# Performance work log

Hardware: AMD Instinct MI355X
Metric: run time of the kernel (lower is better)

Reference implementation:

```python
import jax, jax.numpy as jnp
import numpy as np

B, S, D = 2, 2048, 1024
H = 16
HD = D // H
SCALE = HD ** (-0.5)


def setup_inputs() -> dict:
    key = jax.random.key(0)
    k1, k2, k3, k4 = jax.random.split(key, 4)
    x = jax.random.normal(k1, (B, S, D), dtype=jnp.float32)
    # nn.Linear-style init scale to keep activations sane
    w_qkv = jax.random.normal(k2, (3 * D, D), dtype=jnp.float32) * (D ** -0.5)
    w_out = jax.random.normal(k3, (D, D), dtype=jnp.float32) * (D ** -0.5)
    b_out = jax.random.normal(k4, (D,), dtype=jnp.float32) * 0.01
    return {"x": x, "w_qkv": w_qkv, "w_out": w_out, "b_out": b_out}


def reference(x, w_qkv, w_out, b_out):
    b, s, d = x.shape
    # qkv projection (no bias): [b, s, 3d]
    qkv = jnp.einsum('bsd,ed->bse', x, w_qkv)
    # Rearrange 'b c (e h hd) -> e b h c hd'
    qkv = qkv.reshape(b, s, 3, H, HD).transpose(2, 0, 3, 1, 4)
    # NOTE: original splits as (v, q, k) in that order
    v, q, k = qkv[0], qkv[1], qkv[2]
    # scale applied after matmul, as in the original
    scores = jnp.einsum('bhqd,bhkd->bhqk', q, k) * SCALE
    attn = jax.nn.softmax(scores, axis=-1)
    o = jnp.einsum('bhqk,bhkd->bhqd', attn, v)
    # 'b h c hd -> b c (h hd)'
    o = o.transpose(0, 2, 1, 3).reshape(b, s, d)
    return jnp.einsum('bsd,ed->bse', o, w_out) + b_out
```

## Files before the change

kernel.cpp:

```cpp
#include <hip/hip_runtime.h>
#include <cstdint>
#include <cstddef>

#define BB 2
#define SS 2048
#define DD 1024
#define HH 16
#define HDIM 64

typedef short bf16x8 __attribute__((ext_vector_type(8)));
typedef short bf16x4 __attribute__((ext_vector_type(4)));
typedef float f32x4 __attribute__((ext_vector_type(4)));
typedef float f32x2 __attribute__((ext_vector_type(2)));

union U4S8 { uint4 u; bf16x8 s; };
union U2S4 { uint2 u; bf16x4 s; unsigned short h[4]; };

#if defined(__HIP_DEVICE_COMPILE__)
# if __has_builtin(__builtin_amdgcn_mfma_f32_16x16x16bf16_1k)
#  define MFMA_PV(a, b, c) __builtin_amdgcn_mfma_f32_16x16x16bf16_1k((a), (b), (c), 0, 0, 0)
# else
#  define MFMA_PV(a, b, c) __builtin_amdgcn_mfma_f32_16x16x16_bf16((a), (b), (c), 0, 0, 0)
# endif
# if __has_builtin(__builtin_amdgcn_exp2f)
#  define EXP2(x) __builtin_amdgcn_exp2f(x)
# else
#  define EXP2(x) exp2f(x)
# endif
#else
# define MFMA_PV(a, b, c) (c)
# define EXP2(x) exp2f(x)
#endif

__device__ __forceinline__ unsigned short f2bf(float f) {
    union { float f; unsigned int u; } c; c.f = f;
    unsigned int u = c.u;
    unsigned int r = (u + 0x7FFFu + ((u >> 16) & 1u)) >> 16;
    return (unsigned short)r;
}

__device__ __forceinline__ void async_cp16(const void* g, void* l) {
    __builtin_amdgcn_global_load_lds(
        (const __attribute__((address_space(1))) void*)g,
        (__attribute__((address_space(3))) void*)l, 16, 0, 0);
}

__global__ __launch_bounds__(256) void cvt_all(
    const float* __restrict__ x, const float* __restrict__ wq,
    const float* __restrict__ wo,
    unsigned short* __restrict__ xb, unsigned short* __restrict__ wqb,
    unsigned short* __restrict__ wob) {
    int i = blockIdx.x * 256 + threadIdx.x;
    const float* in; unsigned short* out; int j;
    if (i < 524288)       { in = x;  out = xb;  j = i; }
    else if (i < 917504)  { in = wq; out = wqb; j = i - 524288; }
    else                  { in = wo; out = wob; j = i - 917504; }
    float4 a = ((const float4*)in)[2 * j];
    float4 b = ((const float4*)in)[2 * j + 1];
    union { uint4 u; unsigned short h[8]; } o;
    o.h[0] = f2bf(a.x); o.h[1] = f2bf(a.y); o.h[2] = f2bf(a.z); o.h[3] = f2bf(a.w);
    o.h[4] = f2bf(b.x); o.h[5] = f2bf(b.y); o.h[6] = f2bf(b.z); o.h[7] = f2bf(b.w);
    ((uint4*)out)[j] = o.u;
}

__global__ __launch_bounds__(256) void gemm_qkv(
    const unsigned short* __restrict__ A,
    const unsigned short* __restrict__ Bw,
    unsigned short* __restrict__ qb, unsigned short* __restrict__ kb,
    unsigned short* __restrict__ vb) {
    const int K = 1024;
    __shared__ unsigned short smem[18432];
    int tid = threadIdx.x;
    int lane = tid & 63, wave = tid >> 6;
    int wm = (wave & 1) * 64, wn = (wave >> 1) * 64;
    int m0 = blockIdx.y * 128, n0 = blockIdx.x * 128;
    int lm = lane & 15, lq = lane >> 4;

    f32x4 acc[4][4] = {};

    int sdst = tid * 8;
    const unsigned short* gA = A  + (size_t)(m0 + (tid >> 2)) * K + (tid & 3) * 8;
    const unsigned short* gB = Bw + (size_t)(n0 + (tid >> 2)) * K + (tid & 3) * 8;

#define GSTAGE(k0, buf) do {                                          \
        async_cp16(gA + (k0),          smem + (buf) + sdst);          \
        async_cp16(gA + 64 * K + (k0), smem + (buf) + 2048 + sdst);   \
        async_cp16(gB + (k0),          smem + (buf) + 4096 + sdst);   \
        async_cp16(gB + 64 * K + (k0), smem + (buf) + 6144 + sdst);   \
    } while (0)

    GSTAGE(0, 0);
    for (int k0 = 0; k0 < K; k0 += 64) {
        #pragma unroll
        for (int hf = 0; hf < 2; hf++) {
            int base = hf ? 8192 : 0;
            int obuf = hf ? 0 : 8192;
            __syncthreads();
            int kn = k0 + 32 + hf * 32;
            if (kn < K) GSTAGE(kn, obuf);
            const unsigned short* As = smem + base;
            const unsigned short* Bs = smem + base + 4096;
            U4S8 af[4], bfx[4];
            #pragma unroll
            for (int i = 0; i < 4; i++) {
                af[i].u  = *(const uint4*)(As + (wm + i * 16 + lm) * 32 + lq * 8);
                bfx[i].u = *(const uint4*)(Bs + (wn + i * 16 + lm) * 32 + lq * 8);
            }
            #pragma unroll
            for (int mi = 0; mi < 4; mi++)
                #pragma unroll
                for (int ni = 0; ni < 4; ni++)
                    acc[mi][ni] = __builtin_amdgcn_mfma_f32_16x16x32_bf16(
                        af[mi].s, bfx[ni].s, acc[mi][ni], 0, 0, 0);
        }
    }
#undef GSTAGE
    __syncthreads();

    unsigned short* Lw = smem + wave * 4608;
    int b = m0 >> 11;
    int s_base = (m0 + wm) & 2047;
    if (n0 < 1024) {
        int h = (n0 + wn) >> 6;
        #pragma unroll
        for (int mi = 0; mi < 4; mi++)
            #pragma unroll
            for (int ni = 0; ni < 4; ni++)
                #pragma unroll
                for (int r = 0; r < 4; r++)
                    Lw[(ni * 16 + lm) * 72 + mi * 16 + lq * 4 + r] =
                        f2bf(acc[mi][ni][r]);
        __builtin_amdgcn_wave_barrier();
        unsigned short* vdst = vb + ((size_t)(b * HH + h) * HDIM) * SS + s_base;
        #pragma unroll
        for (int it = 0; it < 8; it++) {
            int hd = it * 8 + (lane >> 3);
            int so = (lane & 7) * 8;
            uint4 val = *(const uint4*)&Lw[hd * 72 + so];
            *(uint4*)(vdst + (size_t)hd * SS + so) = val;
        }
    } else {
        bool isq = n0 < 2048;
        unsigned short* dst = isq ? qb : kb;
        float scale = isq ? 0.18033688f : 1.0f;
        int h = ((n0 + wn) >> 6) & 15;
        #pragma unroll
        for (int mi = 0; mi < 4; mi++)
            #pragma unroll
            for (int ni = 0; ni < 4; ni++)
                #pragma unroll
                for (int r = 0; r < 4; r++)
                    Lw[(mi * 16 + lq * 4 + r) * 72 + ni * 16 + lm] =
                        f2bf(acc[mi][ni][r] * scale);
        __builtin_amdgcn_wave_barrier();
        unsigned short* qdst =
            dst + ((size_t)(b * HH + h) * SS + s_base) * HDIM;
        #pragma unroll
        for (int it = 0; it < 8; it++) {
            int srw = it * 8 + (lane >> 3);
            int so = (lane & 7) * 8;
            uint4 val = *(const uint4*)&Lw[srw * 72 + so];
            *(uint4*)(qdst + (size_t)srw * HDIM + so) = val;
        }
    }
}

__global__ __launch_bounds__(256) void attn(
    const unsigned short* __restrict__ qb,
    const unsigned short* __restrict__ kb,
    const unsigned short* __restrict__ vb,
    unsigned short* __restrict__ ob) {
    int bh = blockIdx.y;
    int q0 = blockIdx.x * 64;
    int tid = threadIdx.x, lane = tid & 63, wave = tid >> 6;
    int lm = lane & 15, lq = lane >> 4;

    __shared__ unsigned short smem[4 * 4096];

    const unsigned short* qg = qb + (size_t)bh * SS * HDIM;
    const unsigned short* kg = kb + (size_t)bh * SS * HDIM;
    const unsigned short* vg = vb + (size_t)bh * HDIM * SS;

    U4S8 qf[2];
    #pragma unroll
    for (int ks = 0; ks < 2; ks++)
        qf[ks].u = *(const uint4*)(
            qg + (size_t)(q0 + wave * 16 + lm) * HDIM + ks * 32 + lq * 8);

    f32x4 oacc[4] = {};
    f32x2 lsum2 = {0.f, 0.f};

    int lm7 = lm & 7;
    int kidx = lm * 64 + 8 * (lq ^ lm7);
    int vidx[4];
    #pragma unroll
    for (int kc = 0; kc < 4; kc++)
        vidx[kc] = lm * 64 + 8 * (((kc << 1) | (lq >> 1)) ^ lm7) + (lq & 1) * 4;

    int srow = tid >> 3;
    int scl  = (tid & 7) ^ (srow & 7);
    int sdst = tid * 8;
    const unsigned short* kptr = kg + (size_t)srow * HDIM + scl * 8;
    const unsigned short* vptr = vg + (size_t)srow * SS + scl * 8;

    #define STAGE(buf)                                                         \
        do {                                                                   \
            async_cp16(kptr,             smem + (buf) + sdst);                 \
            async_cp16(kptr + 32 * HDIM, smem + (buf) + 2048 + sdst);          \
            async_cp16(vptr,             smem + (buf) + 4096 + sdst);          \
            async_cp16(vptr + 32 * SS,   smem + (buf) + 6144 + sdst);          \
            kptr += 64 * HDIM; vptr += 64;                                     \
        } while (0)

    STAGE(0);

    for (int kt = 0; kt < SS / 64; kt += 2) {
        #pragma unroll
        for (int hf = 0; hf < 2; hf++) {
            int base = hf ? 8192 : 0;
            int obuf = hf ? 0 : 8192;
            __syncthreads();
            STAGE(obuf);

            U2S4 pb[4];
            #pragma unroll
            for (int mi = 0; mi < 4; mi++) {
                U4S8 kf0, kf1;
                kf0.u = *(const uint4*)(smem + base + mi * 1024 + kidx);
                kf1.u = *(const uint4*)(smem + base + mi * 1024 + (kidx ^ 32));
                f32x4 sa = {};
                sa = __builtin_amdgcn_mfma_f32_16x16x32_bf16(kf0.s, qf[0].s, sa, 0, 0, 0);
                sa = __builtin_amdgcn_mfma_f32_16x16x32_bf16(kf1.s, qf[1].s, sa, 0, 0, 0);
                float p0 = EXP2(sa[0]);
                float p1 = EXP2(sa[1]);
                float p2 = EXP2(sa[2]);
                float p3 = EXP2(sa[3]);
                f32x2 a01; a01[0] = p0; a01[1] = p1;
                f32x2 a23; a23[0] = p2; a23[1] = p3;
                lsum2 += a01;
                lsum2 += a23;
                unsigned int b0 = __float_as_uint(p0) + 0x8000u;
                unsigned int b1 = __float_as_uint(p1) + 0x8000u;
                unsigned int b2 = __float_as_uint(p2) + 0x8000u;
                unsigned int b3 = __float_as_uint(p3) + 0x8000u;
                pb[mi].u.x = __builtin_amdgcn_perm(b1, b0, 0x07060302u);
                pb[mi].u.y = __builtin_amdgcn_perm(b3, b2, 0x07060302u);
            }

            #pragma unroll
            for (int mi2 = 0; mi2 < 4; mi2++) {
                #pragma unroll
                for (int kc = 0; kc < 4; kc++) {
                    U2S4 vf;
                    vf.u = *(const uint2*)(smem + base + 4096 + mi2 * 1024 + vidx[kc]);
                    oacc[mi2] = MFMA_PV(vf.s, pb[kc].s, oacc[mi2]);
                }
            }
        }
    }
    #undef STAGE

    float s = lsum2[0] + lsum2[1];
    s += __shfl_xor(s, 16);
    s += __shfl_xor(s, 32);
    float inv = 1.f / s;

    __syncthreads();
    unsigned short* Ow = smem + wave * (16 * 72);
    #pragma unroll
    for (int mi2 = 0; mi2 < 4; mi2++) {
        U2S4 t;
        #pragma unroll
        for (int r = 0; r < 4; r++)
            t.h[r] = f2bf(oacc[mi2][r] * inv);
        *(uint2*)&Ow[lm * 72 + mi2 * 16 + lq * 4] = t.u;
    }
    __builtin_amdgcn_wave_barrier();
    int b = bh >> 4, h = bh & 15;
    #pragma unroll
    for (int it = 0; it < 2; it++) {
        int q  = it * 8 + (lane >> 3);
        int off = (lane & 7) * 8;
        uint4 val = *(const uint4*)&Ow[q * 72 + off];
        int srw = q0 + wave * 16 + q;
        *(uint4*)(ob + (size_t)(b * SS + srw) * DD + h * 64 + off) = val;
    }
}

__global__ __launch_bounds__(256) void gemm_out(
    const unsigned short* __restrict__ A,
    const unsigned short* __restrict__ Bw,
    const float* __restrict__ bias, float* __restrict__ out) {
    const int K = 1024;
    __shared__ unsigned short smem[12288];
    int tid = threadIdx.x;
    int lane = tid & 63, wave = tid >> 6;
    int wm = (wave & 1) * 64, wn = (wave >> 1) * 32;
    int m0 = blockIdx.y * 128, n0 = blockIdx.x * 64;
    int lm = lane & 15, lq = lane >> 4;

    f32x4 acc[4][2] = {};

    int sdst = tid * 8;
    const unsigned short* gA = A  + (size_t)(m0 + (tid >> 2)) * K + (tid & 3) * 8;
    const unsigned short* gB = Bw + (size_t)(n0 + (tid >> 2)) * K + (tid & 3) * 8;

#define OSTAGE(k0, buf) do {                                          \
        async_cp16(gA + (k0),          smem + (buf) + sdst);          \
        async_cp16(gA + 64 * K + (k0), smem + (buf) + 2048 + sdst);   \
        async_cp16(gB + (k0),          smem + (buf) + 4096 + sdst);   \
    } while (0)

    OSTAGE(0, 0);
    for (int k0 = 0; k0 < K; k0 += 64) {
        #pragma unroll
        for (int hf = 0; hf < 2; hf++) {
            int base = hf ? 6144 : 0;
            int obuf = hf ? 0 : 6144;
            __syncthreads();
            int kn = k0 + 32 + hf * 32;
            if (kn < K) OSTAGE(kn, obuf);
            const unsigned short* As = smem + base;
            const unsigned short* Bs = smem + base + 4096;
            U4S8 af[4], bfx[2];
            #pragma unroll
            for (int i = 0; i < 4; i++)
                af[i].u = *(const uint4*)(As + (wm + i * 16 + lm) * 32 + lq * 8);
            #pragma unroll
            for (int i = 0; i < 2; i++)
                bfx[i].u = *(const uint4*)(Bs + (wn + i * 16 + lm) * 32 + lq * 8);
            #pragma unroll
            for (int mi = 0; mi < 4; mi++)
                #pragma unroll
                for (int ni = 0; ni < 2; ni++)
                    acc[mi][ni] = __builtin_amdgcn_mfma_f32_16x16x32_bf16(
                        af[mi].s, bfx[ni].s, acc[mi][ni], 0, 0, 0);
        }
    }
#undef OSTAGE

    #pragma unroll
    for (int mi = 0; mi < 4; mi++) {
        int gr = m0 + wm + mi * 16 + lq * 4;
        #pragma unroll
        for (int ni = 0; ni < 2; ni++) {
            int gc = n0 + wn + ni * 16 + lm;
            float bv = bias[gc];
            #pragma unroll
            for (int r = 0; r < 4; r++)
                out[(size_t)(gr + r) * DD + gc] = acc[mi][ni][r] + bv;
        }
    }
}

extern "C" void kernel_launch(void* const* d_in, const int* in_sizes, int n_in,
                              void* d_out, int out_size, void* d_ws, size_t ws_size,
                              hipStream_t stream) {
    const float* x     = (const float*)d_in[0];
    const float* w_qkv = (const float*)d_in[1];
    const float* w_out = (const float*)d_in[2];
    const float* b_out = (const float*)d_in[3];
    float* out = (float*)d_out;

    unsigned short* ws = (unsigned short*)d_ws;
    const size_t NX = (size_t)BB * SS * DD;
    unsigned short* x_bf    = ws;
    unsigned short* wqkv_bf = x_bf + NX;
    unsigned short* wout_bf = wqkv_bf + 3145728;
    unsigned short* q_buf   = wout_bf + 1048576;
    unsigned short* k_buf   = q_buf + NX;
    unsigned short* v_buf   = k_buf + NX;
    unsigned short* o_buf   = v_buf + NX;

    cvt_all<<<4096, 256, 0, stream>>>(x, w_qkv, w_out, x_bf, wqkv_bf, wout_bf);
    gemm_qkv<<<dim3(24, 32), 256, 0, stream>>>(x_bf, wqkv_bf, q_buf, k_buf, v_buf);
    attn<<<dim3(32, 32), 256, 0, stream>>>(q_buf, k_buf, v_buf, o_buf);
    gemm_out<<<dim3(16, 32), 256, 0, stream>>>(o_buf, wout_bf, b_out, out);
}
```

Baseline: 206.6 us.

## Process two query tiles per wave in attention to reuse K/V fragments

Each attention block now covers 128 queries instead of 64, with every wave owning two 16-row query tiles. The K and V fragments loaded from shared memory are reused for both tiles, so the global K/V staging traffic and the LDS reads per query are halved. The grid shrinks to 512 blocks. The cost is more accumulator and probability registers per thread, which may lower occupancy, and fewer blocks to spread across the CUs.

Measured after the change: 205.0 us. About the same (-0.8%).

```diff
diff --git a/kernel.cpp b/kernel.cpp
--- a/kernel.cpp
+++ b/kernel.cpp
@@ -171,7 +171,7 @@
     const unsigned short* __restrict__ vb,
     unsigned short* __restrict__ ob) {
     int bh = blockIdx.y;
-    int q0 = blockIdx.x * 64;
+    int q0 = blockIdx.x * 128;
     int tid = threadIdx.x, lane = tid & 63, wave = tid >> 6;
     int lm = lane & 15, lq = lane >> 4;
 
@@ -181,14 +181,16 @@
     const unsigned short* kg = kb + (size_t)bh * SS * HDIM;
     const unsigned short* vg = vb + (size_t)bh * HDIM * SS;
 
-    U4S8 qf[2];
-    #pragma unroll
-    for (int ks = 0; ks < 2; ks++)
-        qf[ks].u = *(const uint4*)(
-            qg + (size_t)(q0 + wave * 16 + lm) * HDIM + ks * 32 + lq * 8);
-
-    f32x4 oacc[4] = {};
-    f32x2 lsum2 = {0.f, 0.f};
+    U4S8 qf[2][2];
+    #pragma unroll
+    for (int qt = 0; qt < 2; qt++)
+        #pragma unroll
+        for (int ks = 0; ks < 2; ks++)
+            qf[qt][ks].u = *(const uint4*)(
+                qg + (size_t)(q0 + wave * 32 + qt * 16 + lm) * HDIM + ks * 32 + lq * 8);
+
+    f32x4 oacc[4][2] = {};
+    f32x2 lsum2[2] = {};
 
     int lm7 = lm & 7;
     int kidx = lm * 64 + 8 * (lq ^ lm7);
@@ -222,29 +224,32 @@
             __syncthreads();
             STAGE(obuf);
 
-            U2S4 pb[4];
+            U2S4 pb[4][2];
             #pragma unroll
             for (int mi = 0; mi < 4; mi++) {
                 U4S8 kf0, kf1;
                 kf0.u = *(const uint4*)(smem + base + mi * 1024 + kidx);
                 kf1.u = *(const uint4*)(smem + base + mi * 1024 + (kidx ^ 32));
-                f32x4 sa = {};
-                sa = __builtin_amdgcn_mfma_f32_16x16x32_bf16(kf0.s, qf[0].s, sa, 0, 0, 0);
-                sa = __builtin_amdgcn_mfma_f32_16x16x32_bf16(kf1.s, qf[1].s, sa, 0, 0, 0);
-                float p0 = EXP2(sa[0]);
-                float p1 = EXP2(sa[1]);
-                float p2 = EXP2(sa[2]);
-                float p3 = EXP2(sa[3]);
-                f32x2 a01; a01[0] = p0; a01[1] = p1;
-                f32x2 a23; a23[0] = p2; a23[1] = p3;
-                lsum2 += a01;
-                lsum2 += a23;
-                unsigned int b0 = __float_as_uint(p0) + 0x8000u;
-                unsigned int b1 = __float_as_uint(p1) + 0x8000u;
-                unsigned int b2 = __float_as_uint(p2) + 0x8000u;
-                unsigned int b3 = __float_as_uint(p3) + 0x8000u;
-                pb[mi].u.x = __builtin_amdgcn_perm(b1, b0, 0x07060302u);
-                pb[mi].u.y = __builtin_amdgcn_perm(b3, b2, 0x07060302u);
+                #pragma unroll
+                for (int qt = 0; qt < 2; qt++) {
+                    f32x4 sa = {};
+                    sa = __builtin_amdgcn_mfma_f32_16x16x32_bf16(kf0.s, qf[qt][0].s, sa, 0, 0, 0);
+                    sa = __builtin_amdgcn_mfma_f32_16x16x32_bf16(kf1.s, qf[qt][1].s, sa, 0, 0, 0);
+                    float p0 = EXP2(sa[0]);
+                    float p1 = EXP2(sa[1]);
+                    float p2 = EXP2(sa[2]);
+                    float p3 = EXP2(sa[3]);
+                    f32x2 a01; a01[0] = p0; a01[1] = p1;
+                    f32x2 a23; a23[0] = p2; a23[1] = p3;
+                    lsum2[qt] += a01;
+                    lsum2[qt] += a23;
+                    unsigned int b0 = __float_as_uint(p0) + 0x8000u;
+                    unsigned int b1 = __float_as_uint(p1) + 0x8000u;
+                    unsigned int b2 = __float_as_uint(p2) + 0x8000u;
+                    unsigned int b3 = __float_as_uint(p3) + 0x8000u;
+                    pb[mi][qt].u.x = __builtin_amdgcn_perm(b1, b0, 0x07060302u);
+                    pb[mi][qt].u.y = __builtin_amdgcn_perm(b3, b2, 0x07060302u);
+                }
             }
 
             #pragma unroll
@@ -253,36 +258,43 @@
                 for (int kc = 0; kc < 4; kc++) {
                     U2S4 vf;
                     vf.u = *(const uint2*)(smem + base + 4096 + mi2 * 1024 + vidx[kc]);
-                    oacc[mi2] = MFMA_PV(vf.s, pb[kc].s, oacc[mi2]);
+                    oacc[mi2][0] = MFMA_PV(vf.s, pb[kc][0].s, oacc[mi2][0]);
+                    oacc[mi2][1] = MFMA_PV(vf.s, pb[kc][1].s, oacc[mi2][1]);
                 }
             }
         }
     }
     #undef STAGE
 
-    float s = lsum2[0] + lsum2[1];
-    s += __shfl_xor(s, 16);
-    s += __shfl_xor(s, 32);
-    float inv = 1.f / s;
+    float inv[2];
+    #pragma unroll
+    for (int qt = 0; qt < 2; qt++) {
+        float s = lsum2[qt][0] + lsum2[qt][1];
+        s += __shfl_xor(s, 16);
+        s += __shfl_xor(s, 32);
+        inv[qt] = 1.f / s;
+    }
 
     __syncthreads();
-    unsigned short* Ow = smem + wave * (16 * 72);
-    #pragma unroll
-    for (int mi2 = 0; mi2 < 4; mi2++) {
-        U2S4 t;
-        #pragma unroll
-        for (int r = 0; r < 4; r++)
-            t.h[r] = f2bf(oacc[mi2][r] * inv);
-        *(uint2*)&Ow[lm * 72 + mi2 * 16 + lq * 4] = t.u;
-    }
+    unsigned short* Ow = smem + wave * (32 * 72);
+    #pragma unroll
+    for (int mi2 = 0; mi2 < 4; mi2++)
+        #pragma unroll
+        for (int qt = 0; qt < 2; qt++) {
+            U2S4 t;
+            #pragma unroll
+            for (int r = 0; r < 4; r++)
+                t.h[r] = f2bf(oacc[mi2][qt][r] * inv[qt]);
+            *(uint2*)&Ow[(qt * 16 + lm) * 72 + mi2 * 16 + lq * 4] = t.u;
+        }
     __builtin_amdgcn_wave_barrier();
     int b = bh >> 4, h = bh & 15;
     #pragma unroll
-    for (int it = 0; it < 2; it++) {
+    for (int it = 0; it < 4; it++) {
         int q  = it * 8 + (lane >> 3);
         int off = (lane & 7) * 8;
         uint4 val = *(const uint4*)&Ow[q * 72 + off];
-        int srw = q0 + wave * 16 + q;
+        int srw = q0 + wave * 32 + q;
         *(uint4*)(ob + (size_t)(b * SS + srw) * DD + h * 64 + off) = val;
     }
 }
@@ -374,6 +386,6 @@
 
     cvt_all<<<4096, 256, 0, stream>>>(x, w_qkv, w_out, x_bf, wqkv_bf, wout_bf);
     gemm_qkv<<<dim3(24, 32), 256, 0, stream>>>(x_bf, wqkv_bf, q_buf, k_buf, v_buf);
-    attn<<<dim3(32, 32), 256, 0, stream>>>(q_buf, k_buf, v_buf, o_buf);
+    attn<<<dim3(16, 32), 256, 0, stream>>>(q_buf, k_buf, v_buf, o_buf);
     gemm_out<<<dim3(16, 32), 256, 0, stream>>>(o_buf, wout_bf, b_out, out);
 }
```
